# Kernel tuning notes

Hardware: AMD Instinct MI355X
Metric: run time of the kernel (lower is better)

The kernel has to match this reference:

```python
import jax, jax.numpy as jnp
import numpy as np

B, S, D, V, N_BLOCKS = 4096, 128, 9, 5, 4


def _pos_encoding(seq_len, dim):
    pos = jnp.arange(seq_len, dtype=jnp.float32)[:, None]
    d = jnp.arange(dim)[None, :]
    angle = pos / jnp.power(10000.0, (2.0 * (d // 2)) / dim).astype(jnp.float32)
    return jnp.where(d % 2 == 0, jnp.sin(angle), jnp.cos(angle))  # [S, D]


def setup_inputs() -> dict:
    key = jax.random.key(0)
    ks = jax.random.split(key, 10)
    sc = 1.0 / np.sqrt(D)
    return {
        "tokens": jax.random.randint(ks[0], (B, S), 0, V),
        "emb": jax.random.normal(ks[1], (V, D), jnp.float32),
        "Wq": jax.random.normal(ks[2], (N_BLOCKS, D, D), jnp.float32) * sc,
        "bq": jax.random.normal(ks[3], (N_BLOCKS, D), jnp.float32) * sc,
        "Wk": jax.random.normal(ks[4], (N_BLOCKS, D, D), jnp.float32) * sc,
        "bk": jax.random.normal(ks[5], (N_BLOCKS, D), jnp.float32) * sc,
        "Wv": jax.random.normal(ks[6], (N_BLOCKS, D, D), jnp.float32) * sc,
        "bv": jax.random.normal(ks[7], (N_BLOCKS, D), jnp.float32) * sc,
        "Wout": jax.random.normal(ks[8], (V, D), jnp.float32) * sc,
        "bout": jax.random.normal(ks[9], (V,), jnp.float32) * sc,
    }


def reference(tokens, emb, Wq, bq, Wk, bk, Wv, bv, Wout, bout):
    seq_len = tokens.shape[1]
    x = emb[tokens] + _pos_encoding(S, D)[:seq_len]  # [B, S, D]
    scale = 1.0 / jnp.sqrt(jnp.asarray(D, x.dtype))
    for i in range(N_BLOCKS):
        # torch Linear: y = x @ W.T + b
        Q = jnp.einsum('bsd,ed->bse', x, Wq[i]) + bq[i]
        K = jnp.einsum('bsd,ed->bse', x, Wk[i]) + bk[i]
        Vv = jnp.einsum('bsd,ed->bse', x, Wv[i]) + bv[i]
        scores = jnp.einsum('bqd,bkd->bqk', Q, K) * scale  # [B, S, S]
        probs = jax.nn.softmax(scores, axis=-1)
        x = jnp.einsum('bqk,bkd->bqd', probs, Vv)
    logits = jnp.einsum('bsd,vd->bsv', x, Wout) + bout  # [B, S, V]
    return jax.nn.log_softmax(logits, axis=-1)
```

## Files before the change

kernel.cpp:

```cpp
#include <hip/hip_runtime.h>
#include <math.h>

constexpr int Bn = 4096;
constexpr int Sn = 128;
constexpr int Dn = 9;
constexpr int Vn = 5;
constexpr int NBn = 4;

typedef float f4 __attribute__((ext_vector_type(4)));
typedef _Float16 h8 __attribute__((ext_vector_type(8)));
typedef __fp16   h2 __attribute__((ext_vector_type(2)));
typedef unsigned u4v __attribute__((ext_vector_type(4)));
typedef short s4v __attribute__((ext_vector_type(4)));

constexpr int KF_OFF = 0;
constexpr int QF_OFF = 10240;
constexpr int VF_OFF = 20480;
constexpr int XB_OFF = 24832;
constexpr int SMEM_BYTES = 30976;

static __device__ __forceinline__ void store_hl_row(short* rowp, const float* v) {
    h2 h01 = __builtin_amdgcn_cvt_pkrtz(v[0], v[1]);
    h2 h23 = __builtin_amdgcn_cvt_pkrtz(v[2], v[3]);
    h2 h45 = __builtin_amdgcn_cvt_pkrtz(v[4], v[5]);
    h2 h67 = __builtin_amdgcn_cvt_pkrtz(v[6], v[7]);
    h2 h8z = __builtin_amdgcn_cvt_pkrtz(v[8], 0.0f);
    h2 l01 = __builtin_amdgcn_cvt_pkrtz(v[0] - (float)h01.x, v[1] - (float)h01.y);
    h2 l23 = __builtin_amdgcn_cvt_pkrtz(v[2] - (float)h23.x, v[3] - (float)h23.y);
    h2 l45 = __builtin_amdgcn_cvt_pkrtz(v[4] - (float)h45.x, v[5] - (float)h45.y);
    h2 l67 = __builtin_amdgcn_cvt_pkrtz(v[6] - (float)h67.x, v[7] - (float)h67.y);
    h2 l8z = __builtin_amdgcn_cvt_pkrtz(v[8] - (float)h8z.x, 0.0f);
    u4v w0 = (u4v){ __builtin_bit_cast(unsigned, h01), __builtin_bit_cast(unsigned, h23),
                    __builtin_bit_cast(unsigned, h45), __builtin_bit_cast(unsigned, h67) };
    u4v w1 = (u4v){ __builtin_bit_cast(unsigned, h8z), 0u, 0u, 0u };
    u4v w2 = (u4v){ __builtin_bit_cast(unsigned, l01), __builtin_bit_cast(unsigned, l23),
                    __builtin_bit_cast(unsigned, l45), __builtin_bit_cast(unsigned, l67) };
    u4v w3 = (u4v){ __builtin_bit_cast(unsigned, l8z), 0u, 0u, 0u };
    u4v* qp = (u4v*)rowp;
    qp[0] = w0; qp[1] = w1; qp[2] = w2; qp[3] = w3;
}

static __device__ __forceinline__ h8 read_quad(const short* base, int row, int quad) {
    return *(const h8*)(base + row * 40 + quad * 8);
}

__global__ __launch_bounds__(256, 4) void bert_kernel(
    const int*   __restrict__ tokens,
    const float* __restrict__ emb,
    const float* __restrict__ Wq, const float* __restrict__ bq,
    const float* __restrict__ Wk, const float* __restrict__ bk,
    const float* __restrict__ Wv, const float* __restrict__ bv,
    const float* __restrict__ Wout, const float* __restrict__ bout,
    float*       __restrict__ out)
{
    __shared__ __align__(16) char smem[SMEM_BYTES];
    short* KF = (short*)(smem + KF_OFF);
    short* QF = (short*)(smem + QF_OFF);
    short* VF = (short*)(smem + VF_OFF);
    float* XB = (float*)(smem + XB_OFF);

    const int b   = blockIdx.x;
    const int tid = threadIdx.x;
    const int t   = tid & 63;
    const int w   = tid >> 6;
    const int col = t & 15;
    const int g   = t >> 4;
    const bool lowhalf = tid < 128;
    const int r = lowhalf ? tid : tid - 128;
    const float qscale = (1.0f / 3.0f) * 1.44269504f;

    if (lowhalf) {
        const float inv_freq[Dn] = {
            1.0f, 1.0f,
            0.1291549665f, 0.1291549665f,
            0.0166810054f, 0.0166810054f,
            0.0021544347f, 0.0021544347f,
            0.0002782559f
        };
        const int tok = tokens[b * Sn + r];
        float xr[9];
        #pragma unroll
        for (int d = 0; d < Dn; ++d) {
            const float a = (float)r * inv_freq[d];
            const float p = (d & 1) ? cosf(a) : sinf(a);
            xr[d] = emb[tok * Dn + d] + p;
        }
        f4* xp = (f4*)&XB[r * 12];
        xp[0] = (f4){xr[0], xr[1], xr[2], xr[3]};
        xp[1] = (f4){xr[4], xr[5], xr[6], xr[7]};
        xp[2] = (f4){xr[8], 0.0f, 0.0f, 0.0f};
    }
    __syncthreads();

    #pragma unroll 1
    for (int it = 0; it < NBn; ++it) {
        {
            const f4* xp = (const f4*)&XB[r * 12];
            f4 a0 = xp[0], a1 = xp[1], a2 = xp[2];
            float x[9] = {a0.x, a0.y, a0.z, a0.w, a1.x, a1.y, a1.z, a1.w, a2.x};
            const float* wv  = Wv + it * 81;
            const float* bvi = bv + it * 9;
            if (lowhalf) {
                const float* wk  = Wk + it * 81;
                const float* bki = bk + it * 9;
                float kv[9];
                #pragma unroll
                for (int e = 0; e < Dn; ++e) {
                    float ak = bki[e];
                    #pragma unroll
                    for (int d = 0; d < Dn; ++d) ak = fmaf(x[d], wk[e * 9 + d], ak);
                    kv[e] = ak;
                }
                store_hl_row(KF + r * 40, kv);
                #pragma unroll
                for (int e = 0; e < 4; ++e) {
                    float av = bvi[e];
                    #pragma unroll
                    for (int d = 0; d < Dn; ++d) av = fmaf(x[d], wv[e * 9 + d], av);
                    VF[e * 136 + r] = __builtin_bit_cast(short, (_Float16)av);
                }
            } else {
                const float* wq  = Wq + it * 81;
                const float* bqi = bq + it * 9;
                float qv[9];
                #pragma unroll
                for (int e = 0; e < Dn; ++e) {
                    float aq = bqi[e];
                    #pragma unroll
                    for (int d = 0; d < Dn; ++d) aq = fmaf(x[d], wq[e * 9 + d], aq);
                    qv[e] = aq * qscale;
                }
                store_hl_row(QF + r * 40, qv);
                #pragma unroll
                for (int e = 4; e < Dn; ++e) {
                    float av = bvi[e];
                    #pragma unroll
                    for (int d = 0; d < Dn; ++d) av = fmaf(x[d], wv[e * 9 + d], av);
                    VF[e * 136 + r] = __builtin_bit_cast(short, (_Float16)av);
                }
            }
        }
        __syncthreads();

        h8 kfr[8];
        #pragma unroll
        for (int kt = 0; kt < 8; ++kt)
            kfr[kt] = read_quad(KF, kt * 16 + col, g);

        h8 vf[4];
        #pragma unroll
        for (int s = 0; s < 4; ++s) {
            const short* p0 = VF + col * 136 + 32 * s + 4 * g;
            s4v va = *(const s4v*)p0;
            s4v vb = *(const s4v*)(p0 + 16);
            vf[s] = __builtin_bit_cast(h8,
                __builtin_shufflevector(va, vb, 0, 1, 2, 3, 4, 5, 6, 7));
        }

        #pragma unroll
        for (int ti = 0; ti < 2; ++ti) {
            const int qt = 2 * w + ti;
            const int q  = qt * 16 + col;
            h8 b1 = read_quad(QF, q, g & 1);
            h8 b2 = read_quad(QF, q, 2 + (g & 1));

            f4 acc[8];
            #pragma unroll
            for (int kt = 0; kt < 8; ++kt) {
                f4 a = __builtin_amdgcn_mfma_f32_16x16x32_f16(kfr[kt], b1, (f4)(0.0f), 0, 0, 0);
                acc[kt] = __builtin_amdgcn_mfma_f32_16x16x32_f16(kfr[kt], b2, a, 0, 0, 0);
            }
            f4 m0 = __builtin_elementwise_max(acc[0], acc[1]);
            f4 m1 = __builtin_elementwise_max(acc[2], acc[3]);
            f4 m2 = __builtin_elementwise_max(acc[4], acc[5]);
            f4 m3 = __builtin_elementwise_max(acc[6], acc[7]);
            f4 m4 = __builtin_elementwise_max(__builtin_elementwise_max(m0, m1),
                                              __builtin_elementwise_max(m2, m3));
            float mx = fmaxf(fmaxf(m4.x, m4.y), fmaxf(m4.z, m4.w));
            mx = fmaxf(mx, __shfl_xor(mx, 16));
            mx = fmaxf(mx, __shfl_xor(mx, 32));

            float sm = 0.0f;
            #pragma unroll
            for (int kt = 0; kt < 8; ++kt)
                #pragma unroll
                for (int rr = 0; rr < 4; ++rr) {
                    float e2 = __builtin_amdgcn_exp2f(acc[kt][rr] - mx);
                    acc[kt][rr] = e2;
                    sm += e2;
                }
            sm += __shfl_xor(sm, 16);
            sm += __shfl_xor(sm, 32);

            f4 oac = (f4)(0.0f);
            #pragma unroll
            for (int s = 0; s < 4; ++s) {
                u4v up = (u4v){
                    __builtin_bit_cast(unsigned, __builtin_amdgcn_cvt_pkrtz(acc[2*s][0],   acc[2*s][1])),
                    __builtin_bit_cast(unsigned, __builtin_amdgcn_cvt_pkrtz(acc[2*s][2],   acc[2*s][3])),
                    __builtin_bit_cast(unsigned, __builtin_amdgcn_cvt_pkrtz(acc[2*s+1][0], acc[2*s+1][1])),
                    __builtin_bit_cast(unsigned, __builtin_amdgcn_cvt_pkrtz(acc[2*s+1][2], acc[2*s+1][3])) };
                oac = __builtin_amdgcn_mfma_f32_16x16x32_f16(vf[s], __builtin_bit_cast(h8, up), oac, 0, 0, 0);
            }
            const float rl = 1.0f / sm;
            oac *= rl;
            if (g < 3)
                *(f4*)&XB[q * 12 + g * 4] = oac;
        }
        __syncthreads();
    }

    if (lowhalf) {
        const f4* xp = (const f4*)&XB[r * 12];
        f4 a0 = xp[0], a1 = xp[1], a2 = xp[2];
        float xr[9] = {a0.x, a0.y, a0.z, a0.w, a1.x, a1.y, a1.z, a1.w, a2.x};
        float lg[Vn];
        #pragma unroll
        for (int v = 0; v < Vn; ++v) {
            float a = bout[v];
            #pragma unroll
            for (int d = 0; d < Dn; ++d) a = fmaf(xr[d], Wout[v * Dn + d], a);
            lg[v] = a;
        }
        float mm = lg[0];
        #pragma unroll
        for (int v = 1; v < Vn; ++v) mm = fmaxf(mm, lg[v]);
        float sum = 0.0f;
        #pragma unroll
        for (int v = 0; v < Vn; ++v)
            sum += __builtin_amdgcn_exp2f((lg[v] - mm) * 1.44269504f);
        const float lse = __builtin_amdgcn_logf(sum) * 0.69314718f + mm;
        float* op = out + ((size_t)b * Sn + r) * Vn;
        #pragma unroll
        for (int v = 0; v < Vn; ++v) op[v] = lg[v] - lse;
    }
}

extern "C" void kernel_launch(void* const* d_in, const int* in_sizes, int n_in,
                              void* d_out, int out_size, void* d_ws, size_t ws_size,
                              hipStream_t stream) {
    const int*   tokens = (const int*)  d_in[0];
    const float* emb    = (const float*)d_in[1];
    const float* Wq     = (const float*)d_in[2];
    const float* bq_    = (const float*)d_in[3];
    const float* Wk     = (const float*)d_in[4];
    const float* bk_    = (const float*)d_in[5];
    const float* Wv     = (const float*)d_in[6];
    const float* bv_    = (const float*)d_in[7];
    const float* Wout   = (const float*)d_in[8];
    const float* bout_  = (const float*)d_in[9];
    float* out = (float*)d_out;

    bert_kernel<<<dim3(Bn), dim3(256), 0, stream>>>(
        tokens, emb, Wq, bq_, Wk, bk_, Wv, bv_, Wout, bout_, out);
}
```

Baseline: 148.9 us.

## Fold Wq·Wk into bilinear form and compute projections with MFMA

```diff
diff --git a/kernel.cpp b/kernel.cpp
--- a/kernel.cpp
+++ b/kernel.cpp
@@ -10,41 +10,24 @@
 typedef float f4 __attribute__((ext_vector_type(4)));
 typedef _Float16 h8 __attribute__((ext_vector_type(8)));
 typedef __fp16   h2 __attribute__((ext_vector_type(2)));
+typedef __fp16   hv8 __attribute__((ext_vector_type(8)));
 typedef unsigned u4v __attribute__((ext_vector_type(4)));
-typedef short s4v __attribute__((ext_vector_type(4)));
-
-constexpr int KF_OFF = 0;
-constexpr int QF_OFF = 10240;
+typedef short    s4v __attribute__((ext_vector_type(4)));
+
+constexpr int B0_OFF = 0;
+constexpr int B1_OFF = 10240;
 constexpr int VF_OFF = 20480;
-constexpr int XB_OFF = 24832;
-constexpr int SMEM_BYTES = 30976;
-
-static __device__ __forceinline__ void store_hl_row(short* rowp, const float* v) {
-    h2 h01 = __builtin_amdgcn_cvt_pkrtz(v[0], v[1]);
-    h2 h23 = __builtin_amdgcn_cvt_pkrtz(v[2], v[3]);
-    h2 h45 = __builtin_amdgcn_cvt_pkrtz(v[4], v[5]);
-    h2 h67 = __builtin_amdgcn_cvt_pkrtz(v[6], v[7]);
-    h2 h8z = __builtin_amdgcn_cvt_pkrtz(v[8], 0.0f);
-    h2 l01 = __builtin_amdgcn_cvt_pkrtz(v[0] - (float)h01.x, v[1] - (float)h01.y);
-    h2 l23 = __builtin_amdgcn_cvt_pkrtz(v[2] - (float)h23.x, v[3] - (float)h23.y);
-    h2 l45 = __builtin_amdgcn_cvt_pkrtz(v[4] - (float)h45.x, v[5] - (float)h45.y);
-    h2 l67 = __builtin_amdgcn_cvt_pkrtz(v[6] - (float)h67.x, v[7] - (float)h67.y);
-    h2 l8z = __builtin_amdgcn_cvt_pkrtz(v[8] - (float)h8z.x, 0.0f);
-    u4v w0 = (u4v){ __builtin_bit_cast(unsigned, h01), __builtin_bit_cast(unsigned, h23),
-                    __builtin_bit_cast(unsigned, h45), __builtin_bit_cast(unsigned, h67) };
-    u4v w1 = (u4v){ __builtin_bit_cast(unsigned, h8z), 0u, 0u, 0u };
-    u4v w2 = (u4v){ __builtin_bit_cast(unsigned, l01), __builtin_bit_cast(unsigned, l23),
-                    __builtin_bit_cast(unsigned, l45), __builtin_bit_cast(unsigned, l67) };
-    u4v w3 = (u4v){ __builtin_bit_cast(unsigned, l8z), 0u, 0u, 0u };
-    u4v* qp = (u4v*)rowp;
-    qp[0] = w0; qp[1] = w1; qp[2] = w2; qp[3] = w3;
+constexpr int MB_OFF = 24832;
+constexpr int VB_OFF = 25856;
+constexpr int SMEM_BYTES = 26880;
+
+static __device__ __forceinline__ void split_hl(float v, short& h, short& l) {
+    _Float16 hv = (_Float16)v;
+    h = __builtin_bit_cast(short, hv);
+    l = __builtin_bit_cast(short, (_Float16)(v - (float)hv));
 }
 
-static __device__ __forceinline__ h8 read_quad(const short* base, int row, int quad) {
-    return *(const h8*)(base + row * 40 + quad * 8);
-}
-
-__global__ __launch_bounds__(256, 4) void bert_kernel(
+__global__ __launch_bounds__(256, 5) void bert_kernel(
     const int*   __restrict__ tokens,
     const float* __restrict__ emb,
     const float* __restrict__ Wq, const float* __restrict__ bq,
@@ -54,10 +37,11 @@
     float*       __restrict__ out)
 {
     __shared__ __align__(16) char smem[SMEM_BYTES];
-    short* KF = (short*)(smem + KF_OFF);
-    short* QF = (short*)(smem + QF_OFF);
-    short* VF = (short*)(smem + VF_OFF);
-    float* XB = (float*)(smem + XB_OFF);
+    short* BUF0 = (short*)(smem + B0_OFF);
+    short* BUF1 = (short*)(smem + B1_OFF);
+    short* VF   = (short*)(smem + VF_OFF);
+    short* MB   = (short*)(smem + MB_OFF);
+    short* VB   = (short*)(smem + VB_OFF);
 
     const int b   = blockIdx.x;
     const int tid = threadIdx.x;
@@ -65,79 +49,120 @@
     const int w   = tid >> 6;
     const int col = t & 15;
     const int g   = t >> 4;
-    const bool lowhalf = tid < 128;
-    const int r = lowhalf ? tid : tid - 128;
     const float qscale = (1.0f / 3.0f) * 1.44269504f;
 
-    if (lowhalf) {
+    if (tid < 128) {
         const float inv_freq[Dn] = {
-            1.0f, 1.0f,
-            0.1291549665f, 0.1291549665f,
-            0.0166810054f, 0.0166810054f,
-            0.0021544347f, 0.0021544347f,
+            1.0f, 1.0f, 0.1291549665f, 0.1291549665f,
+            0.0166810054f, 0.0166810054f, 0.0021544347f, 0.0021544347f,
             0.0002782559f
         };
+        const int r = tid;
         const int tok = tokens[b * Sn + r];
-        float xr[9];
+        unsigned short sl[32];
         #pragma unroll
         for (int d = 0; d < Dn; ++d) {
             const float a = (float)r * inv_freq[d];
             const float p = (d & 1) ? cosf(a) : sinf(a);
-            xr[d] = emb[tok * Dn + d] + p;
-        }
-        f4* xp = (f4*)&XB[r * 12];
-        xp[0] = (f4){xr[0], xr[1], xr[2], xr[3]};
-        xp[1] = (f4){xr[4], xr[5], xr[6], xr[7]};
-        xp[2] = (f4){xr[8], 0.0f, 0.0f, 0.0f};
+            const float xv = emb[tok * Dn + d] + p;
+            short hh, ll; split_hl(xv, hh, ll);
+            sl[d] = (unsigned short)hh;
+            sl[9 + d] = (unsigned short)ll;
+            sl[18 + d] = (unsigned short)hh;
+        }
+        #pragma unroll
+        for (int d = 27; d < 32; ++d) sl[d] = 0;
+        unsigned wb[16];
+        #pragma unroll
+        for (int j = 0; j < 16; ++j)
+            wb[j] = (unsigned)sl[2 * j] | ((unsigned)sl[2 * j + 1] << 16);
+        u4v* rp = (u4v*)(BUF0 + r * 40);
+        rp[0] = (u4v){wb[0], wb[1], wb[2], wb[3]};
+        rp[1] = (u4v){wb[4], wb[5], wb[6], wb[7]};
+        rp[2] = (u4v){wb[8], wb[9], wb[10], wb[11]};
+        rp[3] = (u4v){wb[12], wb[13], wb[14], wb[15]};
+    } else if (tid < 144) {
+        const int n = tid - 128;
+        MB[n * 32 + 27] = 0;
+        *(unsigned*)(MB + n * 32 + 28) = 0u;
+        *(unsigned*)(MB + n * 32 + 30) = 0u;
+    } else if (tid < 160) {
+        const int n = tid - 144;
+        VB[n * 32 + 27] = 0;
+        *(unsigned*)(VB + n * 32 + 28) = 0u;
+        *(unsigned*)(VB + n * 32 + 30) = 0u;
     }
-    __syncthreads();
 
     #pragma unroll 1
     for (int it = 0; it < NBn; ++it) {
+        short* Xb = (it & 1) ? BUF1 : BUF0;
+        short* Gb = (it & 1) ? BUF0 : BUF1;
+
         {
-            const f4* xp = (const f4*)&XB[r * 12];
-            f4 a0 = xp[0], a1 = xp[1], a2 = xp[2];
-            float x[9] = {a0.x, a0.y, a0.z, a0.w, a1.x, a1.y, a1.z, a1.w, a2.x};
+            const float* wq  = Wq + it * 81;
+            const float* wk  = Wk + it * 81;
             const float* wv  = Wv + it * 81;
+            const float* bqi = bq + it * 9;
+            if (tid < 90) {
+                const int d = tid % 9, n = tid / 9;
+                float a = 0.0f;
+                if (n < 9) {
+                    #pragma unroll
+                    for (int e = 0; e < 9; ++e) a = fmaf(wq[e * 9 + d], wk[e * 9 + n], a);
+                } else {
+                    #pragma unroll
+                    for (int e = 0; e < 9; ++e) a = fmaf(wk[e * 9 + d], bqi[e], a);
+                }
+                a *= qscale;
+                short hh, ll; split_hl(a, hh, ll);
+                MB[n * 32 + d] = hh; MB[n * 32 + 9 + d] = hh; MB[n * 32 + 18 + d] = ll;
+            }
+            if (tid >= 96 && tid < 177) {
+                const int j = tid - 96, d = j % 9, e = j / 9;
+                short hh, ll; split_hl(wv[e * 9 + d], hh, ll);
+                VB[e * 32 + d] = hh; VB[e * 32 + 9 + d] = hh; VB[e * 32 + 18 + d] = ll;
+            }
+        }
+        __syncthreads();
+
+        {
             const float* bvi = bv + it * 9;
-            if (lowhalf) {
-                const float* wk  = Wk + it * 81;
-                const float* bki = bk + it * 9;
-                float kv[9];
-                #pragma unroll
-                for (int e = 0; e < Dn; ++e) {
-                    float ak = bki[e];
-                    #pragma unroll
-                    for (int d = 0; d < Dn; ++d) ak = fmaf(x[d], wk[e * 9 + d], ak);
-                    kv[e] = ak;
+            h8 mbf = *(const h8*)(MB + col * 32 + g * 8);
+            h8 vbf = *(const h8*)(VB + col * 32 + g * 8);
+            const float bvv = (col < 9) ? bvi[col] : 0.0f;
+            f4 cinit = {bvv, bvv, bvv, bvv};
+            #pragma unroll
+            for (int ti = 0; ti < 2; ++ti) {
+                const int mt = 2 * w + ti;
+                h8 xa = *(const h8*)(Xb + (mt * 16 + col) * 40 + g * 8);
+                f4 gt = __builtin_amdgcn_mfma_f32_16x16x32_f16(xa, mbf, (f4)(0.0f), 0, 0, 0);
+                f4 vt = __builtin_amdgcn_mfma_f32_16x16x32_f16(xa, vbf, cinit, 0, 0, 0);
+                const int r0 = mt * 16 + 4 * g;
+                if (col < 9) {
+                    #pragma unroll
+                    for (int rr = 0; rr < 4; ++rr) {
+                        VF[col * 136 + r0 + rr] = __builtin_bit_cast(short, (_Float16)vt[rr]);
+                        short hh, ll; split_hl(gt[rr], hh, ll);
+                        short* rowp = Gb + (r0 + rr) * 40;
+                        rowp[col] = hh; rowp[9 + col] = hh; rowp[18 + col] = ll;
+                    }
+                } else if (col == 9) {
+                    #pragma unroll
+                    for (int rr = 0; rr < 4; ++rr) {
+                        short hh, ll; split_hl(gt[rr], hh, ll);
+                        unsigned pk = (unsigned)(unsigned short)hh
+                                    | ((unsigned)(unsigned short)ll << 16);
+                        *(unsigned*)(Xb + (r0 + rr) * 40 + 30) = pk;
+                    }
+                } else if (col == 10) {
+                    #pragma unroll
+                    for (int rr = 0; rr < 4; ++rr) {
+                        short* rowp = Gb + (r0 + rr) * 40;
+                        rowp[27] = 0;
+                        *(unsigned*)(rowp + 28) = 0u;
+                        *(unsigned*)(rowp + 30) = 0x3C003C00u;
+                    }
                 }
-                store_hl_row(KF + r * 40, kv);
-                #pragma unroll
-                for (int e = 0; e < 4; ++e) {
-                    float av = bvi[e];
-                    #pragma unroll
-                    for (int d = 0; d < Dn; ++d) av = fmaf(x[d], wv[e * 9 + d], av);
-                    VF[e * 136 + r] = __builtin_bit_cast(short, (_Float16)av);
-                }
-            } else {
-                const float* wq  = Wq + it * 81;
-                const float* bqi = bq + it * 9;
-                float qv[9];
-                #pragma unroll
-                for (int e = 0; e < Dn; ++e) {
-                    float aq = bqi[e];
-                    #pragma unroll
-                    for (int d = 0; d < Dn; ++d) aq = fmaf(x[d], wq[e * 9 + d], aq);
-                    qv[e] = aq * qscale;
-                }
-                store_hl_row(QF + r * 40, qv);
-                #pragma unroll
-                for (int e = 4; e < Dn; ++e) {
-                    float av = bvi[e];
-                    #pragma unroll
-                    for (int d = 0; d < Dn; ++d) av = fmaf(x[d], wv[e * 9 + d], av);
-                    VF[e * 136 + r] = __builtin_bit_cast(short, (_Float16)av);
-                }
             }
         }
         __syncthreads();
@@ -145,31 +170,29 @@
         h8 kfr[8];
         #pragma unroll
         for (int kt = 0; kt < 8; ++kt)
-            kfr[kt] = read_quad(KF, kt * 16 + col, g);
-
-        h8 vf[4];
+            kfr[kt] = *(const h8*)(Xb + (kt * 16 + col) * 40 + g * 8);
+
+        h8 vfr[4];
         #pragma unroll
         for (int s = 0; s < 4; ++s) {
             const short* p0 = VF + col * 136 + 32 * s + 4 * g;
             s4v va = *(const s4v*)p0;
-            s4v vb = *(const s4v*)(p0 + 16);
-            vf[s] = __builtin_bit_cast(h8,
-                __builtin_shufflevector(va, vb, 0, 1, 2, 3, 4, 5, 6, 7));
+            s4v vb2 = *(const s4v*)(p0 + 16);
+            vfr[s] = __builtin_bit_cast(h8,
+                __builtin_shufflevector(va, vb2, 0, 1, 2, 3, 4, 5, 6, 7));
         }
 
         #pragma unroll
         for (int ti = 0; ti < 2; ++ti) {
             const int qt = 2 * w + ti;
             const int q  = qt * 16 + col;
-            h8 b1 = read_quad(QF, q, g & 1);
-            h8 b2 = read_quad(QF, q, 2 + (g & 1));
+            h8 bg = *(const h8*)(Gb + q * 40 + g * 8);
 
             f4 acc[8];
             #pragma unroll
-            for (int kt = 0; kt < 8; ++kt) {
-                f4 a = __builtin_amdgcn_mfma_f32_16x16x32_f16(kfr[kt], b1, (f4)(0.0f), 0, 0, 0);
-                acc[kt] = __builtin_amdgcn_mfma_f32_16x16x32_f16(kfr[kt], b2, a, 0, 0, 0);
-            }
+            for (int kt = 0; kt < 8; ++kt)
+                acc[kt] = __builtin_amdgcn_mfma_f32_16x16x32_f16(kfr[kt], bg, (f4)(0.0f), 0, 0, 0);
+
             f4 m0 = __builtin_elementwise_max(acc[0], acc[1]);
             f4 m1 = __builtin_elementwise_max(acc[2], acc[3]);
             f4 m2 = __builtin_elementwise_max(acc[4], acc[5]);
@@ -200,26 +223,54 @@
                     __builtin_bit_cast(unsigned, __builtin_amdgcn_cvt_pkrtz(acc[2*s][2],   acc[2*s][3])),
                     __builtin_bit_cast(unsigned, __builtin_amdgcn_cvt_pkrtz(acc[2*s+1][0], acc[2*s+1][1])),
                     __builtin_bit_cast(unsigned, __builtin_amdgcn_cvt_pkrtz(acc[2*s+1][2], acc[2*s+1][3])) };
-                oac = __builtin_amdgcn_mfma_f32_16x16x32_f16(vf[s], __builtin_bit_cast(h8, up), oac, 0, 0, 0);
+                oac = __builtin_amdgcn_mfma_f32_16x16x32_f16(vfr[s], __builtin_bit_cast(h8, up), oac, 0, 0, 0);
             }
             const float rl = 1.0f / sm;
             oac *= rl;
-            if (g < 3)
-                *(f4*)&XB[q * 12 + g * 4] = oac;
-        }
-        __syncthreads();
+
+            if (g < 2) {
+                h2 p01 = __builtin_amdgcn_cvt_pkrtz(oac.x, oac.y);
+                h2 p23 = __builtin_amdgcn_cvt_pkrtz(oac.z, oac.w);
+                short* rowp = Gb + q * 40;
+                *(unsigned*)(rowp + 4 * g)          = __builtin_bit_cast(unsigned, p01);
+                *(unsigned*)(rowp + 4 * g + 2)      = __builtin_bit_cast(unsigned, p23);
+                *(unsigned*)(rowp + 18 + 4 * g)     = __builtin_bit_cast(unsigned, p01);
+                *(unsigned*)(rowp + 18 + 4 * g + 2) = __builtin_bit_cast(unsigned, p23);
+                rowp[9 + 4 * g + 0] = __builtin_bit_cast(short, (_Float16)(oac.x - (float)p01.x));
+                rowp[9 + 4 * g + 1] = __builtin_bit_cast(short, (_Float16)(oac.y - (float)p01.y));
+                rowp[9 + 4 * g + 2] = __builtin_bit_cast(short, (_Float16)(oac.z - (float)p23.x));
+                rowp[9 + 4 * g + 3] = __builtin_bit_cast(short, (_Float16)(oac.w - (float)p23.y));
+            } else if (g == 2) {
+                short hh, ll; split_hl(oac.x, hh, ll);
+                short* rowp = Gb + q * 40;
+                rowp[8] = hh; rowp[17] = ll; rowp[26] = hh;
+            }
+        }
     }
-
-    if (lowhalf) {
-        const f4* xp = (const f4*)&XB[r * 12];
-        f4 a0 = xp[0], a1 = xp[1], a2 = xp[2];
-        float xr[9] = {a0.x, a0.y, a0.z, a0.w, a1.x, a1.y, a1.z, a1.w, a2.x};
+    __syncthreads();
+
+    if (tid < 128) {
+        const int r = tid;
+        const short* rowp = BUF0 + r * 40;
+        hv8 ha = __builtin_bit_cast(hv8, *(const u4v*)rowp);
+        hv8 hb = __builtin_bit_cast(hv8, *(const u4v*)(rowp + 8));
+        h2  hc = __builtin_bit_cast(h2, *(const unsigned*)(rowp + 16));
+        float x[9];
+        x[0] = (float)ha[0] + (float)hb[1];
+        x[1] = (float)ha[1] + (float)hb[2];
+        x[2] = (float)ha[2] + (float)hb[3];
+        x[3] = (float)ha[3] + (float)hb[4];
+        x[4] = (float)ha[4] + (float)hb[5];
+        x[5] = (float)ha[5] + (float)hb[6];
+        x[6] = (float)ha[6] + (float)hb[7];
+        x[7] = (float)ha[7] + (float)hc.x;
+        x[8] = (float)hb[0] + (float)hc.y;
         float lg[Vn];
         #pragma unroll
         for (int v = 0; v < Vn; ++v) {
             float a = bout[v];
             #pragma unroll
-            for (int d = 0; d < Dn; ++d) a = fmaf(xr[d], Wout[v * Dn + d], a);
+            for (int d = 0; d < Dn; ++d) a = fmaf(x[d], Wout[v * Dn + d], a);
             lg[v] = a;
         }
         float mm = lg[0];
```

New measurement: 174.9 us. +17.5%, slower.
